# Performance work log

Measured on AMD Instinct MI355X. Metric: run time of the kernel, lower is better.

Reference implementation:

```python
import jax, jax.numpy as jnp
import numpy as np

B, S, H = 64, 2048, 512
NEG = -1e9

def setup_inputs() -> dict:
    key = jax.random.key(0)
    k1, k2, k3, k4, k5 = jax.random.split(key, 5)
    encoder_outputs = jax.random.normal(k1, (B, S, H), dtype=jnp.float32)
    mask = jax.random.randint(k2, (B, S), 0, 2).astype(bool)
    W = jax.random.normal(k3, (H, H), dtype=jnp.float32) / np.sqrt(H)
    b = jnp.zeros((H,), dtype=jnp.float32)
    v = jax.random.normal(k4, (H,), dtype=jnp.float32)  # context_vector
    return {"encoder_outputs": encoder_outputs, "mask": mask, "W": W, "b": b, "v": v}

def reference(encoder_outputs, mask, W, b, v):
    # u = tanh(x @ W^T + b): [B,S,H]
    u = jnp.tanh(jnp.einsum('bsh,oh->bso', encoder_outputs, W) + b)
    scores = jnp.einsum('bsh,h->bs', u, v)                 # [B,S]
    scores = jnp.where(mask, scores, NEG)
    attn_weights = jax.nn.softmax(scores, axis=1)          # [B,S]
    weighted_output = jnp.einsum('bsh,bs->bh', encoder_outputs, attn_weights)
    return weighted_output, attn_weights
```

## Files before the change

kernel.cpp:

```cpp
#include <hip/hip_runtime.h>
#include <hip/hip_fp16.h>
#include <stdint.h>

#define NEG_ (-1e9f)

typedef _Float16 f16x8 __attribute__((ext_vector_type(8)));
typedef float    f32x4 __attribute__((ext_vector_type(4)));

__device__ __forceinline__ float fast_tanh(float x) {
  float e = __expf(2.0f * x);
  return (e - 1.0f) * __builtin_amdgcn_rcpf(e + 1.0f);
}

__global__ __launch_bounds__(256) void k0_cvt_w(const float* __restrict__ W,
                                                __half* __restrict__ Wws) {
  int g = blockIdx.x * 256 + threadIdx.x;
  int lane = g & 63;
  int seg  = g >> 6;
  int io = seg & 3, ks = (seg >> 2) & 15, w = (seg >> 6) & 3, oc = seg >> 8;
  int o = oc * 256 + w * 64 + io * 16 + (lane & 15);
  int k = ks * 32 + (lane >> 4) * 8;
  const float2* src = (const float2*)(W + (size_t)o * 512 + k);
  __half2 h[4];
#pragma unroll
  for (int j = 0; j < 4; ++j) { float2 f = src[j]; h[j] = __floats2half2_rn(f.x, f.y); }
  uint4 u;
  u.x = *(uint32_t*)&h[0]; u.y = *(uint32_t*)&h[1];
  u.z = *(uint32_t*)&h[2]; u.w = *(uint32_t*)&h[3];
  *(uint4*)(Wws + (size_t)seg * 512 + (size_t)lane * 8) = u;
}

__global__ __launch_bounds__(256, 2) void k1_scores(
    const float* __restrict__ enc, const int* __restrict__ msk,
    const float* __restrict__ bias, const float* __restrict__ ctx,
    const __half* __restrict__ Wws, float* __restrict__ scores) {
  __shared__ __align__(16) __half Xl[64 * 512];

  const int t = threadIdx.x;
  const int w = t >> 6;
  const int lane = t & 63;
  const int quad = lane >> 4;
  const int l15 = lane & 15;
  const size_t mtile = blockIdx.x;

  {
    const float4* Xg = (const float4*)(enc + mtile * (size_t)(64 * 512));
#pragma unroll
    for (int j = 0; j < 16; ++j) {
      int g = j * 256 + t;
      int s = g >> 6, c = g & 63;
      float4 x0 = Xg[s * 128 + 2 * c];
      float4 x1 = Xg[s * 128 + 2 * c + 1];
      __half2 h0 = __floats2half2_rn(x0.x, x0.y);
      __half2 h1 = __floats2half2_rn(x0.z, x0.w);
      __half2 h2 = __floats2half2_rn(x1.x, x1.y);
      __half2 h3 = __floats2half2_rn(x1.z, x1.w);
      uint4 u;
      u.x = *(uint32_t*)&h0; u.y = *(uint32_t*)&h1;
      u.z = *(uint32_t*)&h2; u.w = *(uint32_t*)&h3;
      int pc = c ^ (s & 7);
      *(uint4*)&Xl[s * 512 + pc * 8] = u;
    }
  }
  __syncthreads();

  float sacc[4] = {0.f, 0.f, 0.f, 0.f};

  f16x8 abuf[3][4];
  auto aload = [&](int slot, int iter) {
    int oc = iter >> 4, ks = iter & 15;
    const f16x8* sp = (const f16x8*)(Wws +
        ((size_t)((oc * 4 + w) * 64 + ks * 4) * 512) + (size_t)lane * 8);
#pragma unroll
    for (int io = 0; io < 4; ++io) abuf[slot][io] = sp[io * 64];
  };
  aload(0, 0);
  aload(1, 1);

#pragma unroll
  for (int oc = 0; oc < 2; ++oc) {
    f32x4 acc[4][4];
#pragma unroll
    for (int io = 0; io < 4; ++io)
#pragma unroll
      for (int is = 0; is < 4; ++is) acc[io][is] = (f32x4){0.f, 0.f, 0.f, 0.f};

#pragma unroll
    for (int ks = 0; ks < 16; ++ks) {
      const int iter = oc * 16 + ks;
      if (iter + 2 < 32) aload((iter + 2) % 3, iter + 2);
      const f16x8* acur = abuf[iter % 3];
#pragma unroll
      for (int is = 0; is < 4; ++is) {
        int s = is * 16 + l15;
        const f16x8 bf = *(const f16x8*)&Xl[s * 512 + (((ks * 4 + quad) ^ (s & 7)) << 3)];
#pragma unroll
        for (int io = 0; io < 4; ++io)
          acc[io][is] = __builtin_amdgcn_mfma_f32_16x16x32_f16(acur[io], bf, acc[io][is], 0, 0, 0);
      }
    }

    float ps[4] = {0.f, 0.f, 0.f, 0.f};
#pragma unroll
    for (int io = 0; io < 4; ++io) {
      int ob = oc * 256 + w * 64 + io * 16 + quad * 4;
      float4 b4 = *(const float4*)(bias + ob);
      float4 v4 = *(const float4*)(ctx + ob);
#pragma unroll
      for (int is = 0; is < 4; ++is) {
        const f32x4 a = acc[io][is];
        ps[is] += fast_tanh(a[0] + b4.x) * v4.x + fast_tanh(a[1] + b4.y) * v4.y +
                  fast_tanh(a[2] + b4.z) * v4.z + fast_tanh(a[3] + b4.w) * v4.w;
      }
    }
#pragma unroll
    for (int is = 0; is < 4; ++is) {
      float p = ps[is];
      p += __shfl_xor(p, 16, 64);
      p += __shfl_xor(p, 32, 64);
      sacc[is] += p;
    }
  }

  __syncthreads();
  float* sred = (float*)&Xl[0];
  if (lane < 16) {
#pragma unroll
    for (int is = 0; is < 4; ++is) sred[w * 64 + is * 16 + lane] = sacc[is];
  }
  __syncthreads();
  if (t < 64) {
    float sc = sred[t] + sred[64 + t] + sred[128 + t] + sred[192 + t];
    size_t row = mtile * 64 + t;
    scores[row] = msk[row] ? sc : NEG_;
  }
}

__global__ __launch_bounds__(256) void k2_softmax(float* __restrict__ attn) {
  const int b = blockIdx.x, t = threadIdx.x;
  float* row = attn + (size_t)b * 2048;
  float v[8];
  float mx = -3.4e38f;
#pragma unroll
  for (int i = 0; i < 8; ++i) { v[i] = row[t + 256 * i]; mx = fmaxf(mx, v[i]); }
#pragma unroll
  for (int off = 32; off >= 1; off >>= 1) mx = fmaxf(mx, __shfl_xor(mx, off, 64));
  __shared__ float r1[4], r2[4];
  int w = t >> 6, lane = t & 63;
  if (lane == 0) r1[w] = mx;
  __syncthreads();
  mx = fmaxf(fmaxf(r1[0], r1[1]), fmaxf(r1[2], r1[3]));
  float sum = 0.f;
#pragma unroll
  for (int i = 0; i < 8; ++i) { v[i] = __expf(v[i] - mx); sum += v[i]; }
#pragma unroll
  for (int off = 32; off >= 1; off >>= 1) sum += __shfl_xor(sum, off, 64);
  if (lane == 0) r2[w] = sum;
  __syncthreads();
  sum = r2[0] + r2[1] + r2[2] + r2[3];
  float inv = 1.0f / sum;
#pragma unroll
  for (int i = 0; i < 8; ++i) row[t + 256 * i] = v[i] * inv;
}

__global__ __launch_bounds__(256) void k3_wsum(const float* __restrict__ enc,
                                               const float* __restrict__ attn,
                                               float* __restrict__ out0) {
  const int bb = blockIdx.x >> 5, sc = blockIdx.x & 31, t = threadIdx.x;
  const int r = t >> 7;
  const int c = t & 127;
  __shared__ float a_s[64];
  if (t < 64) a_s[t] = attn[(size_t)bb * 2048 + sc * 64 + t];
  __syncthreads();
  const float4* Xg = (const float4*)(enc + ((size_t)bb * 2048 + (size_t)sc * 64) * 512);
  float4 acc = {0.f, 0.f, 0.f, 0.f};
#pragma unroll 8
  for (int s = r; s < 64; s += 2) {
    float a = a_s[s];
    float4 x = Xg[(size_t)s * 128 + c];
    acc.x = fmaf(a, x.x, acc.x);
    acc.y = fmaf(a, x.y, acc.y);
    acc.z = fmaf(a, x.z, acc.z);
    acc.w = fmaf(a, x.w, acc.w);
  }
  float* op = out0 + (size_t)bb * 512 + c * 4;
  atomicAdd(op + 0, acc.x);
  atomicAdd(op + 1, acc.y);
  atomicAdd(op + 2, acc.z);
  atomicAdd(op + 3, acc.w);
}

extern "C" void kernel_launch(void* const* d_in, const int* in_sizes, int n_in,
                              void* d_out, int out_size, void* d_ws, size_t ws_size,
                              hipStream_t stream) {
  (void)in_sizes; (void)n_in; (void)out_size; (void)ws_size;
  const float* enc  = (const float*)d_in[0];
  const int*   msk  = (const int*)d_in[1];
  const float* W    = (const float*)d_in[2];
  const float* bias = (const float*)d_in[3];
  const float* ctx  = (const float*)d_in[4];
  float* out0 = (float*)d_out;
  float* attn = out0 + 64 * 512;
  __half* Wws = (__half*)d_ws;

  hipMemsetAsync(out0, 0, 64 * 512 * sizeof(float), stream);
  k0_cvt_w<<<128, 256, 0, stream>>>(W, Wws);
  k1_scores<<<2048, 256, 0, stream>>>(enc, msk, bias, ctx, Wws, attn);
  k2_softmax<<<64, 256, 0, stream>>>(attn);
  k3_wsum<<<2048, 256, 0, stream>>>(enc, attn, out0);
}
```

Baseline: 530.2 us.

## Split k1 output columns across 8 waves and pre-reduce k3 partials before atomics

The scores kernel now runs 512 threads per block, with 8 waves each owning 64 output features. Previously 4 waves each looped over two 256-feature chunks. The W workspace layout is rewritten to match, and the final reduction sums 8 wave partials. This raises per-block parallelism and shortens each wave's serial MFMA chain, at the cost of more register and LDS pressure per block. k3 now combines its two row-halves in shared memory before issuing atomics, which halves the atomic traffic.

```diff
diff --git a/kernel.cpp b/kernel.cpp
--- a/kernel.cpp
+++ b/kernel.cpp
@@ -17,8 +17,8 @@
   int g = blockIdx.x * 256 + threadIdx.x;
   int lane = g & 63;
   int seg  = g >> 6;
-  int io = seg & 3, ks = (seg >> 2) & 15, w = (seg >> 6) & 3, oc = seg >> 8;
-  int o = oc * 256 + w * 64 + io * 16 + (lane & 15);
+  int io = seg & 3, ks = (seg >> 2) & 15, w = seg >> 6;
+  int o = w * 64 + io * 16 + (lane & 15);
   int k = ks * 32 + (lane >> 4) * 8;
   const float2* src = (const float2*)(W + (size_t)o * 512 + k);
   __half2 h[4];
@@ -30,7 +30,7 @@
   *(uint4*)(Wws + (size_t)seg * 512 + (size_t)lane * 8) = u;
 }
 
-__global__ __launch_bounds__(256, 2) void k1_scores(
+__global__ __launch_bounds__(512, 4) void k1_scores(
     const float* __restrict__ enc, const int* __restrict__ msk,
     const float* __restrict__ bias, const float* __restrict__ ctx,
     const __half* __restrict__ Wws, float* __restrict__ scores) {
@@ -46,8 +46,8 @@
   {
     const float4* Xg = (const float4*)(enc + mtile * (size_t)(64 * 512));
 #pragma unroll
-    for (int j = 0; j < 16; ++j) {
-      int g = j * 256 + t;
+    for (int j = 0; j < 8; ++j) {
+      int g = j * 512 + t;
       int s = g >> 6, c = g & 63;
       float4 x0 = Xg[s * 128 + 2 * c];
       float4 x1 = Xg[s * 128 + 2 * c + 1];
@@ -64,73 +64,66 @@
   }
   __syncthreads();
 
-  float sacc[4] = {0.f, 0.f, 0.f, 0.f};
-
   f16x8 abuf[3][4];
-  auto aload = [&](int slot, int iter) {
-    int oc = iter >> 4, ks = iter & 15;
+  auto aload = [&](int slot, int ks) {
     const f16x8* sp = (const f16x8*)(Wws +
-        ((size_t)((oc * 4 + w) * 64 + ks * 4) * 512) + (size_t)lane * 8);
+        ((size_t)(w * 64 + ks * 4) * 512) + (size_t)lane * 8);
 #pragma unroll
     for (int io = 0; io < 4; ++io) abuf[slot][io] = sp[io * 64];
   };
   aload(0, 0);
   aload(1, 1);
 
-#pragma unroll
-  for (int oc = 0; oc < 2; ++oc) {
-    f32x4 acc[4][4];
-#pragma unroll
-    for (int io = 0; io < 4; ++io)
-#pragma unroll
-      for (int is = 0; is < 4; ++is) acc[io][is] = (f32x4){0.f, 0.f, 0.f, 0.f};
-
-#pragma unroll
-    for (int ks = 0; ks < 16; ++ks) {
-      const int iter = oc * 16 + ks;
-      if (iter + 2 < 32) aload((iter + 2) % 3, iter + 2);
-      const f16x8* acur = abuf[iter % 3];
-#pragma unroll
-      for (int is = 0; is < 4; ++is) {
-        int s = is * 16 + l15;
-        const f16x8 bf = *(const f16x8*)&Xl[s * 512 + (((ks * 4 + quad) ^ (s & 7)) << 3)];
-#pragma unroll
-        for (int io = 0; io < 4; ++io)
-          acc[io][is] = __builtin_amdgcn_mfma_f32_16x16x32_f16(acur[io], bf, acc[io][is], 0, 0, 0);
-      }
+  f32x4 acc[4][4];
+#pragma unroll
+  for (int io = 0; io < 4; ++io)
+#pragma unroll
+    for (int is = 0; is < 4; ++is) acc[io][is] = (f32x4){0.f, 0.f, 0.f, 0.f};
+
+#pragma unroll
+  for (int ks = 0; ks < 16; ++ks) {
+    if (ks + 2 < 16) aload((ks + 2) % 3, ks + 2);
+    const f16x8* acur = abuf[ks % 3];
+#pragma unroll
+    for (int is = 0; is < 4; ++is) {
+      int s = is * 16 + l15;
+      const f16x8 bf = *(const f16x8*)&Xl[s * 512 + (((ks * 4 + quad) ^ (s & 7)) << 3)];
+#pragma unroll
+      for (int io = 0; io < 4; ++io)
+        acc[io][is] = __builtin_amdgcn_mfma_f32_16x16x32_f16(acur[io], bf, acc[io][is], 0, 0, 0);
     }
-
-    float ps[4] = {0.f, 0.f, 0.f, 0.f};
-#pragma unroll
-    for (int io = 0; io < 4; ++io) {
-      int ob = oc * 256 + w * 64 + io * 16 + quad * 4;
-      float4 b4 = *(const float4*)(bias + ob);
-      float4 v4 = *(const float4*)(ctx + ob);
-#pragma unroll
-      for (int is = 0; is < 4; ++is) {
-        const f32x4 a = acc[io][is];
-        ps[is] += fast_tanh(a[0] + b4.x) * v4.x + fast_tanh(a[1] + b4.y) * v4.y +
-                  fast_tanh(a[2] + b4.z) * v4.z + fast_tanh(a[3] + b4.w) * v4.w;
-      }
+  }
+
+  float ps[4] = {0.f, 0.f, 0.f, 0.f};
+#pragma unroll
+  for (int io = 0; io < 4; ++io) {
+    int ob = w * 64 + io * 16 + quad * 4;
+    float4 b4 = *(const float4*)(bias + ob);
+    float4 v4 = *(const float4*)(ctx + ob);
+#pragma unroll
+    for (int is = 0; is < 4; ++is) {
+      const f32x4 a = acc[io][is];
+      ps[is] += fast_tanh(a[0] + b4.x) * v4.x + fast_tanh(a[1] + b4.y) * v4.y +
+                fast_tanh(a[2] + b4.z) * v4.z + fast_tanh(a[3] + b4.w) * v4.w;
     }
-#pragma unroll
-    for (int is = 0; is < 4; ++is) {
-      float p = ps[is];
-      p += __shfl_xor(p, 16, 64);
-      p += __shfl_xor(p, 32, 64);
-      sacc[is] += p;
-    }
+  }
+#pragma unroll
+  for (int is = 0; is < 4; ++is) {
+    ps[is] += __shfl_xor(ps[is], 16, 64);
+    ps[is] += __shfl_xor(ps[is], 32, 64);
   }
 
   __syncthreads();
   float* sred = (float*)&Xl[0];
   if (lane < 16) {
 #pragma unroll
-    for (int is = 0; is < 4; ++is) sred[w * 64 + is * 16 + lane] = sacc[is];
+    for (int is = 0; is < 4; ++is) sred[w * 64 + is * 16 + lane] = ps[is];
   }
   __syncthreads();
   if (t < 64) {
-    float sc = sred[t] + sred[64 + t] + sred[128 + t] + sred[192 + t];
+    float sc = 0.f;
+#pragma unroll
+    for (int k = 0; k < 8; ++k) sc += sred[k * 64 + t];
     size_t row = mtile * 64 + t;
     scores[row] = msk[row] ? sc : NEG_;
   }
@@ -170,6 +163,7 @@
   const int r = t >> 7;
   const int c = t & 127;
   __shared__ float a_s[64];
+  __shared__ __align__(16) float4 part[128];
   if (t < 64) a_s[t] = attn[(size_t)bb * 2048 + sc * 64 + t];
   __syncthreads();
   const float4* Xg = (const float4*)(enc + ((size_t)bb * 2048 + (size_t)sc * 64) * 512);
@@ -183,11 +177,16 @@
     acc.z = fmaf(a, x.z, acc.z);
     acc.w = fmaf(a, x.w, acc.w);
   }
-  float* op = out0 + (size_t)bb * 512 + c * 4;
-  atomicAdd(op + 0, acc.x);
-  atomicAdd(op + 1, acc.y);
-  atomicAdd(op + 2, acc.z);
-  atomicAdd(op + 3, acc.w);
+  if (r) part[c] = acc;
+  __syncthreads();
+  if (!r) {
+    float4 o = part[c];
+    float* op = out0 + (size_t)bb * 512 + c * 4;
+    atomicAdd(op + 0, acc.x + o.x);
+    atomicAdd(op + 1, acc.y + o.y);
+    atomicAdd(op + 2, acc.z + o.z);
+    atomicAdd(op + 3, acc.w + o.w);
+  }
 }
 
 extern "C" void kernel_launch(void* const* d_in, const int* in_sizes, int n_in,
@@ -205,7 +204,7 @@
 
   hipMemsetAsync(out0, 0, 64 * 512 * sizeof(float), stream);
   k0_cvt_w<<<128, 256, 0, stream>>>(W, Wws);
-  k1_scores<<<2048, 256, 0, stream>>>(enc, msk, bias, ctx, Wws, attn);
+  k1_scores<<<2048, 512, 0, stream>>>(enc, msk, bias, ctx, Wws, attn);
   k2_softmax<<<64, 256, 0, stream>>>(attn);
   k3_wsum<<<2048, 256, 0, stream>>>(enc, attn, out0);
 }
```

Result: faster. 517.1 us (-2.5%).
